# Kernel tuning notes

Measured on AMD Instinct MI355X. Metric: run time of the kernel, lower is better.

## Reference

```python
import jax, jax.numpy as jnp
import numpy as np

NUM_HEADS = 4
SCALE = 0.1767766952966369  # head_dim**-0.5, head_dim=32


def setup_inputs() -> dict:
    key = jax.random.key(0)
    k1, k2, k3 = jax.random.split(key, 3)
    B, N, C = 4096, 49, 384  # B = 64 images * 64 windows, N = 7*7, C = 3*embed_dims
    qkv = jax.random.normal(k1, (B, N, C), dtype=jnp.float32)
    mask = jax.random.normal(k2, (NUM_HEADS, N, N), dtype=jnp.float32)
    rotate_mask = jax.random.normal(k3, (64, N, N), dtype=jnp.float32)  # nW = 64
    hw_pad = jnp.array([56, 56], dtype=jnp.int32)  # metadata only, unused in math
    return {"qkv": qkv, "mask": mask, "rotate_mask": rotate_mask, "hw_pad": hw_pad}


def reference(qkv, mask, rotate_mask, hw_pad):
    B, N, C = qkv.shape
    H = NUM_HEADS
    hd = C // H // 3
    # [B,N,3,H,hd] -> [3,B,H,N,hd]
    qkv_r = qkv.reshape(B, N, 3, H, hd).transpose(2, 0, 3, 1, 4)
    q, k, v = qkv_r[0] * SCALE, qkv_r[1], qkv_r[2]
    attn = jnp.einsum('bhqd,bhkd->bhqk', q, k) + mask  # mask broadcasts over B
    nW = rotate_mask.shape[0]
    # shifted-window mask: add per-window rotate mask, broadcast over image batch and heads
    attn = attn.reshape(B // nW, nW, H, N, N) + rotate_mask[None, :, None, :, :]
    attn = jax.nn.softmax(attn.reshape(B, H, N, N), axis=-1)
    out = jnp.einsum('bhqk,bhkd->bhqd', attn, v)  # [B,H,N,hd]
    return out.transpose(0, 2, 1, 3).reshape(B, N, C // 3)
```

## Files before the change

### kernel.cpp

```cpp
#include <hip/hip_runtime.h>

#define NTOK 49
#define NH 4
#define HD 32
#define CIN 384
#define NW 64
#define NPAD 64
#define SCALE_F 0.1767766952966369f

typedef _Float16 f16x8 __attribute__((ext_vector_type(8)));
typedef float f32x16 __attribute__((ext_vector_type(16)));
typedef __fp16 fp16x2 __attribute__((ext_vector_type(2)));

__device__ __forceinline__ unsigned int pkh(float a, float b) {
    fp16x2 h = __builtin_amdgcn_cvt_pkrtz(a, b);
    return __builtin_bit_cast(unsigned int, h);
}

__global__ __launch_bounds__(64) void prep_cmask(
    const float* __restrict__ mask,
    const float* __restrict__ rot,
    float* __restrict__ cmT)
{
    const int wh = blockIdx.x;
    const int w = wh >> 2, h = wh & 3;
    const int i = threadIdx.x;
    for (int j = 0; j < NPAD; ++j) {
        float v;
        if (j >= NTOK) v = -1e30f;
        else if (i >= NTOK) v = 0.f;
        else v = mask[(h * NTOK + i) * NTOK + j] + rot[(w * NTOK + i) * NTOK + j];
        cmT[((size_t)wh * NPAD + j) * NPAD + i] = v;
    }
}

template<bool USE_CM>
__global__ __launch_bounds__(128) void win_attn_mfma(
    const float* __restrict__ qkv,
    const float* __restrict__ mask,
    const float* __restrict__ rot,
    const float* __restrict__ cmT,
    float* __restrict__ out)
{
    const int h = blockIdx.x & 3;
    const int b = blockIdx.x >> 2;
    const int w = b & (NW - 1);
    const int tid = threadIdx.x;
    const int it = tid >> 6;
    const int lane = tid & 63;
    const int l31 = lane & 31;
    const int hl = lane >> 5;

    __shared__ _Float16 Qs[NPAD * HD];
    __shared__ _Float16 Ks[NPAD * HD];

    const float* base = qkv + (size_t)b * (NTOK * CIN) + h * HD;

    #pragma unroll
    for (int t4 = 0; t4 < 4; ++t4) {
        const int idx = tid + t4 * 128;
        const int n = idx >> 3;
        const int c = idx & 7;
        float4 fq = make_float4(0.f, 0.f, 0.f, 0.f);
        float4 fk = fq;
        if (n < NTOK) {
            const float* p = base + n * CIN + c * 4;
            fq = *reinterpret_cast<const float4*>(p);
            fk = *reinterpret_cast<const float4*>(p + 128);
        }
        uint2 uq, uk;
        uq.x = pkh(fq.x * SCALE_F, fq.y * SCALE_F);
        uq.y = pkh(fq.z * SCALE_F, fq.w * SCALE_F);
        uk.x = pkh(fk.x, fk.y);
        uk.y = pkh(fk.z, fk.w);
        *reinterpret_cast<uint2*>(&Qs[n * HD + c * 4]) = uq;
        *reinterpret_cast<uint2*>(&Ks[n * HD + c * 4]) = uk;
    }

    const int i = l31 + 32 * it;
    float cm[2][16];
    #pragma unroll
    for (int jt = 0; jt < 2; ++jt) {
        #pragma unroll
        for (int r = 0; r < 16; ++r) {
            const int j = (r & 3) + 8 * (r >> 2) + 4 * hl + 32 * jt;
            if (USE_CM) {
                cm[jt][r] = cmT[((size_t)(w * 4 + h) * NPAD + j) * NPAD + i];
            } else {
                float v;
                if (j >= NTOK) v = -1e30f;
                else if (i >= NTOK) v = 0.f;
                else v = mask[(h * NTOK + i) * NTOK + j] + rot[(w * NTOK + i) * NTOK + j];
                cm[jt][r] = v;
            }
        }
    }

    __syncthreads();

    f16x8 ka[2][2], qa[2];
    #pragma unroll
    for (int t = 0; t < 2; ++t) {
        #pragma unroll
        for (int ks = 0; ks < 2; ++ks) {
            ka[t][ks] = *reinterpret_cast<const f16x8*>(&Ks[(l31 + 32 * t) * HD + ks * 16 + hl * 8]);
        }
    }
    #pragma unroll
    for (int ks = 0; ks < 2; ++ks) {
        qa[ks] = *reinterpret_cast<const f16x8*>(&Qs[(l31 + 32 * it) * HD + ks * 16 + hl * 8]);
    }

    f32x16 acc[2];
    #pragma unroll
    for (int jt = 0; jt < 2; ++jt) {
        f32x16 a;
        #pragma unroll
        for (int r = 0; r < 16; ++r) a[r] = 0.f;
        a = __builtin_amdgcn_mfma_f32_32x32x16_f16(ka[jt][0], qa[0], a, 0, 0, 0);
        a = __builtin_amdgcn_mfma_f32_32x32x16_f16(ka[jt][1], qa[1], a, 0, 0, 0);
        acc[jt] = a;
    }

    float m = -3e38f;
    #pragma unroll
    for (int jt = 0; jt < 2; ++jt) {
        #pragma unroll
        for (int r = 0; r < 16; ++r) {
            acc[jt][r] += cm[jt][r];
            m = fmaxf(m, acc[jt][r]);
        }
    }
    m = fmaxf(m, __shfl_xor(m, 32));
    float s = 0.f;
    #pragma unroll
    for (int jt = 0; jt < 2; ++jt) {
        #pragma unroll
        for (int r = 0; r < 16; ++r) {
            const float e = __expf(acc[jt][r] - m);
            acc[jt][r] = e;
            s += e;
        }
    }
    s += __shfl_xor(s, 32);
    const float inv = 1.f / s;
    #pragma unroll
    for (int jt = 0; jt < 2; ++jt) {
        #pragma unroll
        for (int r = 0; r < 16; ++r) acc[jt][r] *= inv;
    }

    f32x16 oacc;
    #pragma unroll
    for (int r = 0; r < 16; ++r) oacc[r] = 0.f;

    #pragma unroll
    for (int ks = 0; ks < 4; ++ks) {
        unsigned int vd[4];
        #pragma unroll
        for (int ep = 0; ep < 4; ++ep) {
            const int j0 = 16 * ks + 8 * hl + 2 * ep;
            float v0 = 0.f, v1 = 0.f;
            if (j0 < NTOK)
                v0 = qkv[((size_t)b * NTOK + j0) * CIN + 256 + h * HD + l31];
            if (j0 + 1 < NTOK)
                v1 = qkv[((size_t)b * NTOK + j0 + 1) * CIN + 256 + h * HD + l31];
            vd[ep] = pkh(v0, v1);
        }
        uint4 vu = make_uint4(vd[0], vd[1], vd[2], vd[3]);
        const f16x8 vb = __builtin_bit_cast(f16x8, vu);

        const int jt = ks >> 1;
        const int r8 = 8 * (ks & 1);
        const unsigned lo0 = pkh(acc[jt][r8 + 0], acc[jt][r8 + 1]);
        const unsigned lo1 = pkh(acc[jt][r8 + 2], acc[jt][r8 + 3]);
        const unsigned hi0 = pkh(acc[jt][r8 + 4], acc[jt][r8 + 5]);
        const unsigned hi1 = pkh(acc[jt][r8 + 6], acc[jt][r8 + 7]);
        const unsigned x0 = hl ? lo0 : hi0;
        const unsigned x1 = hl ? lo1 : hi1;
        const unsigned y0 = (unsigned)__shfl_xor((int)x0, 32);
        const unsigned y1 = (unsigned)__shfl_xor((int)x1, 32);
        uint4 pu;
        pu.x = hl ? y0 : lo0;
        pu.y = hl ? y1 : lo1;
        pu.z = hl ? hi0 : y0;
        pu.w = hl ? hi1 : y1;
        const f16x8 pa = __builtin_bit_cast(f16x8, pu);
        oacc = __builtin_amdgcn_mfma_f32_32x32x16_f16(pa, vb, oacc, 0, 0, 0);
    }

    float* obase = out + (size_t)b * NTOK * (NH * HD) + h * HD + l31;
    #pragma unroll
    for (int r = 0; r < 16; ++r) {
        const int io = (r & 3) + 8 * (r >> 2) + 4 * hl + 32 * it;
        if (io < NTOK) obase[(size_t)io * (NH * HD)] = oacc[r];
    }
}

extern "C" void kernel_launch(void* const* d_in, const int* in_sizes, int n_in,
                              void* d_out, int out_size, void* d_ws, size_t ws_size,
                              hipStream_t stream) {
    const float* qkv  = (const float*)d_in[0];
    const float* mask = (const float*)d_in[1];
    const float* rot  = (const float*)d_in[2];
    float* out = (float*)d_out;

    const int Btot = in_sizes[0] / (NTOK * CIN);
    dim3 grid(Btot * NH);

    const size_t cm_bytes = (size_t)NW * NH * NPAD * NPAD * sizeof(float);
    if (ws_size >= cm_bytes && d_ws != nullptr) {
        float* cmT = (float*)d_ws;
        prep_cmask<<<dim3(NW * NH), 64, 0, stream>>>(mask, rot, cmT);
        win_attn_mfma<true><<<grid, 128, 0, stream>>>(qkv, mask, rot, cmT, out);
    } else {
        win_attn_mfma<false><<<grid, 128, 0, stream>>>(qkv, mask, rot, nullptr, out);
    }
}
```

Measured before the change: 106.9 us.

## Make attention blocks persistent over 8 problems with double-buffered Q/K staging

Each block now handles 8 consecutive (window, head) problems instead of one. Q/K for the next problem are loaded and converted into a second LDS buffer while the current one computes. V loads are hoisted ahead of the softmax so their latency overlaps the QK MFMA. The aim is to hide global load latency and cut block launch overhead, at the cost of fewer blocks (16384 → 2048), more registers and a serialized per-block loop.

```diff
diff --git a/kernel.cpp b/kernel.cpp
--- a/kernel.cpp
+++ b/kernel.cpp
@@ -6,6 +6,7 @@
 #define CIN 384
 #define NW 64
 #define NPAD 64
+#define NPER 8
 #define SCALE_F 0.1767766952966369f
 
 typedef _Float16 f16x8 __attribute__((ext_vector_type(8)));
@@ -40,160 +41,184 @@
     const float* __restrict__ mask,
     const float* __restrict__ rot,
     const float* __restrict__ cmT,
-    float* __restrict__ out)
+    float* __restrict__ out,
+    int nprob)
 {
-    const int h = blockIdx.x & 3;
-    const int b = blockIdx.x >> 2;
-    const int w = b & (NW - 1);
     const int tid = threadIdx.x;
     const int it = tid >> 6;
     const int lane = tid & 63;
     const int l31 = lane & 31;
     const int hl = lane >> 5;
 
-    __shared__ _Float16 Qs[NPAD * HD];
-    __shared__ _Float16 Ks[NPAD * HD];
-
-    const float* base = qkv + (size_t)b * (NTOK * CIN) + h * HD;
-
-    #pragma unroll
-    for (int t4 = 0; t4 < 4; ++t4) {
-        const int idx = tid + t4 * 128;
-        const int n = idx >> 3;
-        const int c = idx & 7;
-        float4 fq = make_float4(0.f, 0.f, 0.f, 0.f);
-        float4 fk = fq;
-        if (n < NTOK) {
-            const float* p = base + n * CIN + c * 4;
-            fq = *reinterpret_cast<const float4*>(p);
-            fk = *reinterpret_cast<const float4*>(p + 128);
-        }
-        uint2 uq, uk;
-        uq.x = pkh(fq.x * SCALE_F, fq.y * SCALE_F);
-        uq.y = pkh(fq.z * SCALE_F, fq.w * SCALE_F);
-        uk.x = pkh(fk.x, fk.y);
-        uk.y = pkh(fk.z, fk.w);
-        *reinterpret_cast<uint2*>(&Qs[n * HD + c * 4]) = uq;
-        *reinterpret_cast<uint2*>(&Ks[n * HD + c * 4]) = uk;
-    }
-
-    const int i = l31 + 32 * it;
-    float cm[2][16];
-    #pragma unroll
-    for (int jt = 0; jt < 2; ++jt) {
+    __shared__ _Float16 Qs[2][NPAD * HD];
+    __shared__ _Float16 Ks[2][NPAD * HD];
+
+    const int p0 = blockIdx.x * NPER;
+
+    auto stage = [&](int p, int s) {
+        const int hh = p & 3;
+        const int bb = p >> 2;
+        const float* base = qkv + (size_t)bb * (NTOK * CIN) + hh * HD;
+        #pragma unroll
+        for (int t4 = 0; t4 < 4; ++t4) {
+            const int idx = tid + t4 * 128;
+            const int n = idx >> 3;
+            const int c = idx & 7;
+            float4 fq = make_float4(0.f, 0.f, 0.f, 0.f);
+            float4 fk = fq;
+            if (n < NTOK) {
+                const float* pp = base + n * CIN + c * 4;
+                fq = *reinterpret_cast<const float4*>(pp);
+                fk = *reinterpret_cast<const float4*>(pp + 128);
+            }
+            uint2 uq, uk;
+            uq.x = pkh(fq.x * SCALE_F, fq.y * SCALE_F);
+            uq.y = pkh(fq.z * SCALE_F, fq.w * SCALE_F);
+            uk.x = pkh(fk.x, fk.y);
+            uk.y = pkh(fk.z, fk.w);
+            *reinterpret_cast<uint2*>(&Qs[s][n * HD + c * 4]) = uq;
+            *reinterpret_cast<uint2*>(&Ks[s][n * HD + c * 4]) = uk;
+        }
+    };
+
+    if (p0 >= nprob) return;
+    stage(p0, 0);
+    __syncthreads();
+
+    int cur = 0;
+    #pragma unroll 1
+    for (int t = 0; t < NPER; ++t) {
+        const int p = p0 + t;
+        if (p >= nprob) break;
+        const int h = p & 3;
+        const int b = p >> 2;
+        const int w = b & (NW - 1);
+        const int i = l31 + 32 * it;
+
+        float cm[2][16];
+        #pragma unroll
+        for (int jt = 0; jt < 2; ++jt) {
+            #pragma unroll
+            for (int r = 0; r < 16; ++r) {
+                const int j = (r & 3) + 8 * (r >> 2) + 4 * hl + 32 * jt;
+                if (USE_CM) {
+                    cm[jt][r] = cmT[((size_t)(w * 4 + h) * NPAD + j) * NPAD + i];
+                } else {
+                    float v;
+                    if (j >= NTOK) v = -1e30f;
+                    else if (i >= NTOK) v = 0.f;
+                    else v = mask[(h * NTOK + i) * NTOK + j] + rot[(w * NTOK + i) * NTOK + j];
+                    cm[jt][r] = v;
+                }
+            }
+        }
+
+        uint4 vb[4];
+        {
+            const float* vbase = qkv + (size_t)b * (NTOK * CIN) + 256 + h * HD + l31;
+            #pragma unroll
+            for (int ks = 0; ks < 4; ++ks) {
+                unsigned dd[4];
+                #pragma unroll
+                for (int ep = 0; ep < 4; ++ep) {
+                    const int j0 = 16 * ks + 8 * hl + 2 * ep;
+                    const float v0 = (j0     < NTOK) ? vbase[(size_t)j0 * CIN]       : 0.f;
+                    const float v1 = (j0 + 1 < NTOK) ? vbase[(size_t)(j0 + 1) * CIN] : 0.f;
+                    dd[ep] = pkh(v0, v1);
+                }
+                vb[ks] = make_uint4(dd[0], dd[1], dd[2], dd[3]);
+            }
+        }
+
+        f16x8 ka[2][2], qa[2];
+        #pragma unroll
+        for (int kt = 0; kt < 2; ++kt) {
+            #pragma unroll
+            for (int ks = 0; ks < 2; ++ks) {
+                ka[kt][ks] = *reinterpret_cast<const f16x8*>(&Ks[cur][(l31 + 32 * kt) * HD + ks * 16 + hl * 8]);
+            }
+        }
+        #pragma unroll
+        for (int ks = 0; ks < 2; ++ks) {
+            qa[ks] = *reinterpret_cast<const f16x8*>(&Qs[cur][(l31 + 32 * it) * HD + ks * 16 + hl * 8]);
+        }
+
+        if (t + 1 < NPER && p + 1 < nprob) stage(p + 1, cur ^ 1);
+
+        f32x16 acc[2];
+        #pragma unroll
+        for (int jt = 0; jt < 2; ++jt) {
+            f32x16 a;
+            #pragma unroll
+            for (int r = 0; r < 16; ++r) a[r] = 0.f;
+            a = __builtin_amdgcn_mfma_f32_32x32x16_f16(ka[jt][0], qa[0], a, 0, 0, 0);
+            a = __builtin_amdgcn_mfma_f32_32x32x16_f16(ka[jt][1], qa[1], a, 0, 0, 0);
+            acc[jt] = a;
+        }
+
+        float m = -3e38f;
+        #pragma unroll
+        for (int jt = 0; jt < 2; ++jt) {
+            #pragma unroll
+            for (int r = 0; r < 16; ++r) {
+                acc[jt][r] += cm[jt][r];
+                m = fmaxf(m, acc[jt][r]);
+            }
+        }
+        m = fmaxf(m, __shfl_xor(m, 32));
+        float s = 0.f;
+        #pragma unroll
+        for (int jt = 0; jt < 2; ++jt) {
+            #pragma unroll
+            for (int r = 0; r < 16; ++r) {
+                const float e = __expf(acc[jt][r] - m);
+                acc[jt][r] = e;
+                s += e;
+            }
+        }
+        s += __shfl_xor(s, 32);
+        const float inv = 1.f / s;
+        #pragma unroll
+        for (int jt = 0; jt < 2; ++jt) {
+            #pragma unroll
+            for (int r = 0; r < 16; ++r) acc[jt][r] *= inv;
+        }
+
+        f32x16 oacc;
+        #pragma unroll
+        for (int r = 0; r < 16; ++r) oacc[r] = 0.f;
+
+        #pragma unroll
+        for (int ks = 0; ks < 4; ++ks) {
+            const int jt = ks >> 1;
+            const int r8 = 8 * (ks & 1);
+            const unsigned lo0 = pkh(acc[jt][r8 + 0], acc[jt][r8 + 1]);
+            const unsigned lo1 = pkh(acc[jt][r8 + 2], acc[jt][r8 + 3]);
+            const unsigned hi0 = pkh(acc[jt][r8 + 4], acc[jt][r8 + 5]);
+            const unsigned hi1 = pkh(acc[jt][r8 + 6], acc[jt][r8 + 7]);
+            const unsigned x0 = hl ? lo0 : hi0;
+            const unsigned x1 = hl ? lo1 : hi1;
+            const unsigned y0 = (unsigned)__shfl_xor((int)x0, 32);
+            const unsigned y1 = (unsigned)__shfl_xor((int)x1, 32);
+            uint4 pu;
+            pu.x = hl ? y0 : lo0;
+            pu.y = hl ? y1 : lo1;
+            pu.z = hl ? hi0 : y0;
+            pu.w = hl ? hi1 : y1;
+            const f16x8 pa  = __builtin_bit_cast(f16x8, pu);
+            const f16x8 vbk = __builtin_bit_cast(f16x8, vb[ks]);
+            oacc = __builtin_amdgcn_mfma_f32_32x32x16_f16(pa, vbk, oacc, 0, 0, 0);
+        }
+
+        float* obase = out + (size_t)b * NTOK * (NH * HD) + h * HD + l31;
         #pragma unroll
         for (int r = 0; r < 16; ++r) {
-            const int j = (r & 3) + 8 * (r >> 2) + 4 * hl + 32 * jt;
-            if (USE_CM) {
-                cm[jt][r] = cmT[((size_t)(w * 4 + h) * NPAD + j) * NPAD + i];
-            } else {
-                float v;
-                if (j >= NTOK) v = -1e30f;
-                else if (i >= NTOK) v = 0.f;
-                else v = mask[(h * NTOK + i) * NTOK + j] + rot[(w * NTOK + i) * NTOK + j];
-                cm[jt][r] = v;
-            }
-        }
-    }
-
-    __syncthreads();
-
-    f16x8 ka[2][2], qa[2];
-    #pragma unroll
-    for (int t = 0; t < 2; ++t) {
-        #pragma unroll
-        for (int ks = 0; ks < 2; ++ks) {
-            ka[t][ks] = *reinterpret_cast<const f16x8*>(&Ks[(l31 + 32 * t) * HD + ks * 16 + hl * 8]);
-        }
-    }
-    #pragma unroll
-    for (int ks = 0; ks < 2; ++ks) {
-        qa[ks] = *reinterpret_cast<const f16x8*>(&Qs[(l31 + 32 * it) * HD + ks * 16 + hl * 8]);
-    }
-
-    f32x16 acc[2];
-    #pragma unroll
-    for (int jt = 0; jt < 2; ++jt) {
-        f32x16 a;
-        #pragma unroll
-        for (int r = 0; r < 16; ++r) a[r] = 0.f;
-        a = __builtin_amdgcn_mfma_f32_32x32x16_f16(ka[jt][0], qa[0], a, 0, 0, 0);
-        a = __builtin_amdgcn_mfma_f32_32x32x16_f16(ka[jt][1], qa[1], a, 0, 0, 0);
-        acc[jt] = a;
-    }
-
-    float m = -3e38f;
-    #pragma unroll
-    for (int jt = 0; jt < 2; ++jt) {
-        #pragma unroll
-        for (int r = 0; r < 16; ++r) {
-            acc[jt][r] += cm[jt][r];
-            m = fmaxf(m, acc[jt][r]);
-        }
-    }
-    m = fmaxf(m, __shfl_xor(m, 32));
-    float s = 0.f;
-    #pragma unroll
-    for (int jt = 0; jt < 2; ++jt) {
-        #pragma unroll
-        for (int r = 0; r < 16; ++r) {
-            const float e = __expf(acc[jt][r] - m);
-            acc[jt][r] = e;
-            s += e;
-        }
-    }
-    s += __shfl_xor(s, 32);
-    const float inv = 1.f / s;
-    #pragma unroll
-    for (int jt = 0; jt < 2; ++jt) {
-        #pragma unroll
-        for (int r = 0; r < 16; ++r) acc[jt][r] *= inv;
-    }
-
-    f32x16 oacc;
-    #pragma unroll
-    for (int r = 0; r < 16; ++r) oacc[r] = 0.f;
-
-    #pragma unroll
-    for (int ks = 0; ks < 4; ++ks) {
-        unsigned int vd[4];
-        #pragma unroll
-        for (int ep = 0; ep < 4; ++ep) {
-            const int j0 = 16 * ks + 8 * hl + 2 * ep;
-            float v0 = 0.f, v1 = 0.f;
-            if (j0 < NTOK)
-                v0 = qkv[((size_t)b * NTOK + j0) * CIN + 256 + h * HD + l31];
-            if (j0 + 1 < NTOK)
-                v1 = qkv[((size_t)b * NTOK + j0 + 1) * CIN + 256 + h * HD + l31];
-            vd[ep] = pkh(v0, v1);
-        }
-        uint4 vu = make_uint4(vd[0], vd[1], vd[2], vd[3]);
-        const f16x8 vb = __builtin_bit_cast(f16x8, vu);
-
-        const int jt = ks >> 1;
-        const int r8 = 8 * (ks & 1);
-        const unsigned lo0 = pkh(acc[jt][r8 + 0], acc[jt][r8 + 1]);
-        const unsigned lo1 = pkh(acc[jt][r8 + 2], acc[jt][r8 + 3]);
-        const unsigned hi0 = pkh(acc[jt][r8 + 4], acc[jt][r8 + 5]);
-        const unsigned hi1 = pkh(acc[jt][r8 + 6], acc[jt][r8 + 7]);
-        const unsigned x0 = hl ? lo0 : hi0;
-        const unsigned x1 = hl ? lo1 : hi1;
-        const unsigned y0 = (unsigned)__shfl_xor((int)x0, 32);
-        const unsigned y1 = (unsigned)__shfl_xor((int)x1, 32);
-        uint4 pu;
-        pu.x = hl ? y0 : lo0;
-        pu.y = hl ? y1 : lo1;
-        pu.z = hl ? hi0 : y0;
-        pu.w = hl ? hi1 : y1;
-        const f16x8 pa = __builtin_bit_cast(f16x8, pu);
-        oacc = __builtin_amdgcn_mfma_f32_32x32x16_f16(pa, vb, oacc, 0, 0, 0);
-    }
-
-    float* obase = out + (size_t)b * NTOK * (NH * HD) + h * HD + l31;
-    #pragma unroll
-    for (int r = 0; r < 16; ++r) {
-        const int io = (r & 3) + 8 * (r >> 2) + 4 * hl + 32 * it;
-        if (io < NTOK) obase[(size_t)io * (NH * HD)] = oacc[r];
+            const int io = (r & 3) + 8 * (r >> 2) + 4 * hl + 32 * it;
+            if (io < NTOK) obase[(size_t)io * (NH * HD)] = oacc[r];
+        }
+
+        __syncthreads();
+        cur ^= 1;
     }
 }
 
@@ -206,14 +231,15 @@
     float* out = (float*)d_out;
 
     const int Btot = in_sizes[0] / (NTOK * CIN);
-    dim3 grid(Btot * NH);
+    const int nprob = Btot * NH;
+    dim3 grid((nprob + NPER - 1) / NPER);
 
     const size_t cm_bytes = (size_t)NW * NH * NPAD * NPAD * sizeof(float);
     if (ws_size >= cm_bytes && d_ws != nullptr) {
         float* cmT = (float*)d_ws;
         prep_cmask<<<dim3(NW * NH), 64, 0, stream>>>(mask, rot, cmT);
-        win_attn_mfma<true><<<grid, 128, 0, stream>>>(qkv, mask, rot, cmT, out);
+        win_attn_mfma<true><<<grid, 128, 0, stream>>>(qkv, mask, rot, cmT, out, nprob);
     } else {
-        win_attn_mfma<false><<<grid, 128, 0, stream>>>(qkv, mask, rot, nullptr, out);
+        win_attn_mfma<false><<<grid, 128, 0, stream>>>(qkv, mask, rot, nullptr, out, nprob);
     }
 }
```

Measured after the change: 123.1 us. 1.15x slower.

## Process all four heads of a window in one 512-thread block

Applied to the files above, without the earlier changes.

Merges the four per-head blocks into one block per window of 8 waves, two per head. The Q and K rows of all heads are staged into padded shared memory (row stride 136 halves) with fully contiguous float4 loads. This cuts the block count fourfold and coalesces the global reads of Q/K across heads. In exchange each block uses more shared memory and larger blocks, which may lower occupancy, and V is still read directly from global memory.

```diff
diff --git a/kernel.cpp b/kernel.cpp
--- a/kernel.cpp
+++ b/kernel.cpp
@@ -6,6 +6,7 @@
 #define CIN 384
 #define NW 64
 #define NPAD 64
+#define QKP 136
 #define SCALE_F 0.1767766952966369f
 
 typedef _Float16 f16x8 __attribute__((ext_vector_type(8)));
@@ -35,46 +36,51 @@
 }
 
 template<bool USE_CM>
-__global__ __launch_bounds__(128) void win_attn_mfma(
+__global__ __launch_bounds__(512) void win_attn_mfma(
     const float* __restrict__ qkv,
     const float* __restrict__ mask,
     const float* __restrict__ rot,
     const float* __restrict__ cmT,
     float* __restrict__ out)
 {
-    const int h = blockIdx.x & 3;
-    const int b = blockIdx.x >> 2;
+    const int b = blockIdx.x;
     const int w = b & (NW - 1);
     const int tid = threadIdx.x;
-    const int it = tid >> 6;
+    const int wid = tid >> 6;
+    const int h = wid >> 1;
+    const int it = wid & 1;
     const int lane = tid & 63;
     const int l31 = lane & 31;
     const int hl = lane >> 5;
 
-    __shared__ _Float16 Qs[NPAD * HD];
-    __shared__ _Float16 Ks[NPAD * HD];
-
-    const float* base = qkv + (size_t)b * (NTOK * CIN) + h * HD;
-
-    #pragma unroll
-    for (int t4 = 0; t4 < 4; ++t4) {
-        const int idx = tid + t4 * 128;
-        const int n = idx >> 3;
-        const int c = idx & 7;
-        float4 fq = make_float4(0.f, 0.f, 0.f, 0.f);
-        float4 fk = fq;
-        if (n < NTOK) {
-            const float* p = base + n * CIN + c * 4;
-            fq = *reinterpret_cast<const float4*>(p);
-            fk = *reinterpret_cast<const float4*>(p + 128);
-        }
-        uint2 uq, uk;
-        uq.x = pkh(fq.x * SCALE_F, fq.y * SCALE_F);
-        uq.y = pkh(fq.z * SCALE_F, fq.w * SCALE_F);
-        uk.x = pkh(fk.x, fk.y);
-        uk.y = pkh(fk.z, fk.w);
-        *reinterpret_cast<uint2*>(&Qs[n * HD + c * 4]) = uq;
-        *reinterpret_cast<uint2*>(&Ks[n * HD + c * 4]) = uk;
+    __shared__ _Float16 Qs[NPAD * QKP];
+    __shared__ _Float16 Ks[NPAD * QKP];
+
+    const float* base = qkv + (size_t)b * (NTOK * CIN);
+
+    for (int e = tid; e < NTOK * 64; e += 512) {
+        const int n = e >> 6;
+        const int c = e & 63;
+        const int col = c * 4;
+        const float4 f = *reinterpret_cast<const float4*>(base + n * CIN + col);
+        uint2 u;
+        if (col < 128) {
+            u.x = pkh(f.x * SCALE_F, f.y * SCALE_F);
+            u.y = pkh(f.z * SCALE_F, f.w * SCALE_F);
+            *reinterpret_cast<uint2*>(&Qs[n * QKP + col]) = u;
+        } else {
+            u.x = pkh(f.x, f.y);
+            u.y = pkh(f.z, f.w);
+            *reinterpret_cast<uint2*>(&Ks[n * QKP + (col - 128)]) = u;
+        }
+    }
+    for (int e = tid; e < 15 * 64; e += 512) {
+        const int n = NTOK + (e >> 6);
+        const int c = e & 63;
+        const int col = c * 4;
+        const uint2 z = make_uint2(0u, 0u);
+        if (col < 128) *reinterpret_cast<uint2*>(&Qs[n * QKP + col]) = z;
+        else           *reinterpret_cast<uint2*>(&Ks[n * QKP + (col - 128)]) = z;
     }
 
     const int i = l31 + 32 * it;
@@ -100,15 +106,15 @@
 
     f16x8 ka[2][2], qa[2];
     #pragma unroll
-    for (int t = 0; t < 2; ++t) {
+    for (int kt = 0; kt < 2; ++kt) {
         #pragma unroll
         for (int ks = 0; ks < 2; ++ks) {
-            ka[t][ks] = *reinterpret_cast<const f16x8*>(&Ks[(l31 + 32 * t) * HD + ks * 16 + hl * 8]);
+            ka[kt][ks] = *reinterpret_cast<const f16x8*>(&Ks[(l31 + 32 * kt) * QKP + h * HD + ks * 16 + hl * 8]);
         }
     }
     #pragma unroll
     for (int ks = 0; ks < 2; ++ks) {
-        qa[ks] = *reinterpret_cast<const f16x8*>(&Qs[(l31 + 32 * it) * HD + ks * 16 + hl * 8]);
+        qa[ks] = *reinterpret_cast<const f16x8*>(&Qs[(l31 + 32 * it) * QKP + h * HD + ks * 16 + hl * 8]);
     }
 
     f32x16 acc[2];
@@ -206,14 +212,14 @@
     float* out = (float*)d_out;
 
     const int Btot = in_sizes[0] / (NTOK * CIN);
-    dim3 grid(Btot * NH);
+    dim3 grid(Btot);
 
     const size_t cm_bytes = (size_t)NW * NH * NPAD * NPAD * sizeof(float);
     if (ws_size >= cm_bytes && d_ws != nullptr) {
         float* cmT = (float*)d_ws;
         prep_cmask<<<dim3(NW * NH), 64, 0, stream>>>(mask, rot, cmT);
-        win_attn_mfma<true><<<grid, 128, 0, stream>>>(qkv, mask, rot, cmT, out);
+        win_attn_mfma<true><<<grid, 512, 0, stream>>>(qkv, mask, rot, cmT, out);
     } else {
-        win_attn_mfma<false><<<grid, 128, 0, stream>>>(qkv, mask, rot, nullptr, out);
-    }
-}
+        win_attn_mfma<false><<<grid, 512, 0, stream>>>(qkv, mask, rot, nullptr, out);
+    }
+}
```

After: 108.2 us. No clear change (+1.2%).

## Process two (window, head) problems per block with prefetch of second Q/K

Applied to the files above, without the earlier changes.

Each block now handles two consecutive (batch, head) attention problems, using double-buffered shared Q/K tiles. The second problem's Q/K are loaded into registers before the first is computed, so global load latency overlaps with the first problem's MFMA and softmax work. This halves the grid size and raises register pressure, and assumes the total problem count is even.

```diff
diff --git a/kernel.cpp b/kernel.cpp
--- a/kernel.cpp
+++ b/kernel.cpp
@@ -42,19 +42,23 @@
     const float* __restrict__ cmT,
     float* __restrict__ out)
 {
-    const int h = blockIdx.x & 3;
-    const int b = blockIdx.x >> 2;
-    const int w = b & (NW - 1);
     const int tid = threadIdx.x;
     const int it = tid >> 6;
     const int lane = tid & 63;
     const int l31 = lane & 31;
     const int hl = lane >> 5;
-
-    __shared__ _Float16 Qs[NPAD * HD];
-    __shared__ _Float16 Ks[NPAD * HD];
-
-    const float* base = qkv + (size_t)b * (NTOK * CIN) + h * HD;
+    const int i = l31 + 32 * it;
+
+    __shared__ _Float16 Qs[2][NPAD * HD];
+    __shared__ _Float16 Ks[2][NPAD * HD];
+
+    const int pA = blockIdx.x * 2;
+    const int pB = pA + 1;
+    const int hA = pA & 3, bA = pA >> 2, wA = bA & (NW - 1);
+    const int hB = pB & 3, bB = pB >> 2, wB = bB & (NW - 1);
+
+    const float* baseA = qkv + (size_t)bA * (NTOK * CIN) + hA * HD;
+    const float* baseB = qkv + (size_t)bB * (NTOK * CIN) + hB * HD;
 
     #pragma unroll
     for (int t4 = 0; t4 < 4; ++t4) {
@@ -64,137 +68,178 @@
         float4 fq = make_float4(0.f, 0.f, 0.f, 0.f);
         float4 fk = fq;
         if (n < NTOK) {
-            const float* p = base + n * CIN + c * 4;
-            fq = *reinterpret_cast<const float4*>(p);
-            fk = *reinterpret_cast<const float4*>(p + 128);
+            const float* pp = baseA + n * CIN + c * 4;
+            fq = *reinterpret_cast<const float4*>(pp);
+            fk = *reinterpret_cast<const float4*>(pp + 128);
         }
         uint2 uq, uk;
         uq.x = pkh(fq.x * SCALE_F, fq.y * SCALE_F);
         uq.y = pkh(fq.z * SCALE_F, fq.w * SCALE_F);
         uk.x = pkh(fk.x, fk.y);
         uk.y = pkh(fk.z, fk.w);
-        *reinterpret_cast<uint2*>(&Qs[n * HD + c * 4]) = uq;
-        *reinterpret_cast<uint2*>(&Ks[n * HD + c * 4]) = uk;
-    }
-
-    const int i = l31 + 32 * it;
-    float cm[2][16];
+        *reinterpret_cast<uint2*>(&Qs[0][n * HD + c * 4]) = uq;
+        *reinterpret_cast<uint2*>(&Ks[0][n * HD + c * 4]) = uk;
+    }
+
+    float4 bq[4], bk[4];
     #pragma unroll
-    for (int jt = 0; jt < 2; ++jt) {
+    for (int t4 = 0; t4 < 4; ++t4) {
+        const int idx = tid + t4 * 128;
+        const int n = idx >> 3;
+        const int c = idx & 7;
+        bq[t4] = make_float4(0.f, 0.f, 0.f, 0.f);
+        bk[t4] = bq[t4];
+        if (n < NTOK) {
+            const float* pp = baseB + n * CIN + c * 4;
+            bq[t4] = *reinterpret_cast<const float4*>(pp);
+            bk[t4] = *reinterpret_cast<const float4*>(pp + 128);
+        }
+    }
+
+    auto load_cm = [&](int w, int h, float cm[2][16]) {
+        #pragma unroll
+        for (int jt = 0; jt < 2; ++jt) {
+            #pragma unroll
+            for (int r = 0; r < 16; ++r) {
+                const int j = (r & 3) + 8 * (r >> 2) + 4 * hl + 32 * jt;
+                if (USE_CM) {
+                    cm[jt][r] = cmT[((size_t)(w * 4 + h) * NPAD + j) * NPAD + i];
+                } else {
+                    float v;
+                    if (j >= NTOK) v = -1e30f;
+                    else if (i >= NTOK) v = 0.f;
+                    else v = mask[(h * NTOK + i) * NTOK + j] + rot[(w * NTOK + i) * NTOK + j];
+                    cm[jt][r] = v;
+                }
+            }
+        }
+    };
+
+    auto compute = [&](int s, int b, int h, const float cm[2][16]) {
+        f16x8 ka[2][2], qa[2];
+        #pragma unroll
+        for (int kt = 0; kt < 2; ++kt) {
+            #pragma unroll
+            for (int ks = 0; ks < 2; ++ks) {
+                ka[kt][ks] = *reinterpret_cast<const f16x8*>(&Ks[s][(l31 + 32 * kt) * HD + ks * 16 + hl * 8]);
+            }
+        }
+        #pragma unroll
+        for (int ks = 0; ks < 2; ++ks) {
+            qa[ks] = *reinterpret_cast<const f16x8*>(&Qs[s][(l31 + 32 * it) * HD + ks * 16 + hl * 8]);
+        }
+
+        f32x16 acc[2];
+        #pragma unroll
+        for (int jt = 0; jt < 2; ++jt) {
+            f32x16 a;
+            #pragma unroll
+            for (int r = 0; r < 16; ++r) a[r] = 0.f;
+            a = __builtin_amdgcn_mfma_f32_32x32x16_f16(ka[jt][0], qa[0], a, 0, 0, 0);
+            a = __builtin_amdgcn_mfma_f32_32x32x16_f16(ka[jt][1], qa[1], a, 0, 0, 0);
+            acc[jt] = a;
+        }
+
+        float m = -3e38f;
+        #pragma unroll
+        for (int jt = 0; jt < 2; ++jt) {
+            #pragma unroll
+            for (int r = 0; r < 16; ++r) {
+                acc[jt][r] += cm[jt][r];
+                m = fmaxf(m, acc[jt][r]);
+            }
+        }
+        m = fmaxf(m, __shfl_xor(m, 32));
+        float sum = 0.f;
+        #pragma unroll
+        for (int jt = 0; jt < 2; ++jt) {
+            #pragma unroll
+            for (int r = 0; r < 16; ++r) {
+                const float e = __expf(acc[jt][r] - m);
+                acc[jt][r] = e;
+                sum += e;
+            }
+        }
+        sum += __shfl_xor(sum, 32);
+        const float inv = 1.f / sum;
+        #pragma unroll
+        for (int jt = 0; jt < 2; ++jt) {
+            #pragma unroll
+            for (int r = 0; r < 16; ++r) acc[jt][r] *= inv;
+        }
+
+        f32x16 oacc;
+        #pragma unroll
+        for (int r = 0; r < 16; ++r) oacc[r] = 0.f;
+
+        #pragma unroll
+        for (int ks = 0; ks < 4; ++ks) {
+            unsigned int vd[4];
+            #pragma unroll
+            for (int ep = 0; ep < 4; ++ep) {
+                const int j0 = 16 * ks + 8 * hl + 2 * ep;
+                float v0 = 0.f, v1 = 0.f;
+                if (j0 < NTOK)
+                    v0 = qkv[((size_t)b * NTOK + j0) * CIN + 256 + h * HD + l31];
+                if (j0 + 1 < NTOK)
+                    v1 = qkv[((size_t)b * NTOK + j0 + 1) * CIN + 256 + h * HD + l31];
+                vd[ep] = pkh(v0, v1);
+            }
+            uint4 vu = make_uint4(vd[0], vd[1], vd[2], vd[3]);
+            const f16x8 vb = __builtin_bit_cast(f16x8, vu);
+
+            const int jt = ks >> 1;
+            const int r8 = 8 * (ks & 1);
+            const unsigned lo0 = pkh(acc[jt][r8 + 0], acc[jt][r8 + 1]);
+            const unsigned lo1 = pkh(acc[jt][r8 + 2], acc[jt][r8 + 3]);
+            const unsigned hi0 = pkh(acc[jt][r8 + 4], acc[jt][r8 + 5]);
+            const unsigned hi1 = pkh(acc[jt][r8 + 6], acc[jt][r8 + 7]);
+            const unsigned x0 = hl ? lo0 : hi0;
+            const unsigned x1 = hl ? lo1 : hi1;
+            const unsigned y0 = (unsigned)__shfl_xor((int)x0, 32);
+            const unsigned y1 = (unsigned)__shfl_xor((int)x1, 32);
+            uint4 pu;
+            pu.x = hl ? y0 : lo0;
+            pu.y = hl ? y1 : lo1;
+            pu.z = hl ? hi0 : y0;
+            pu.w = hl ? hi1 : y1;
+            const f16x8 pa = __builtin_bit_cast(f16x8, pu);
+            oacc = __builtin_amdgcn_mfma_f32_32x32x16_f16(pa, vb, oacc, 0, 0, 0);
+        }
+
+        float* obase = out + (size_t)b * NTOK * (NH * HD) + h * HD + l31;
         #pragma unroll
         for (int r = 0; r < 16; ++r) {
-            const int j = (r & 3) + 8 * (r >> 2) + 4 * hl + 32 * jt;
-            if (USE_CM) {
-                cm[jt][r] = cmT[((size_t)(w * 4 + h) * NPAD + j) * NPAD + i];
-            } else {
-                float v;
-                if (j >= NTOK) v = -1e30f;
-                else if (i >= NTOK) v = 0.f;
-                else v = mask[(h * NTOK + i) * NTOK + j] + rot[(w * NTOK + i) * NTOK + j];
-                cm[jt][r] = v;
-            }
-        }
-    }
+            const int io = (r & 3) + 8 * (r >> 2) + 4 * hl + 32 * it;
+            if (io < NTOK) obase[(size_t)io * (NH * HD)] = oacc[r];
+        }
+    };
+
+    float cmA[2][16];
+    load_cm(wA, hA, cmA);
 
     __syncthreads();
-
-    f16x8 ka[2][2], qa[2];
+    compute(0, bA, hA, cmA);
+
     #pragma unroll
-    for (int t = 0; t < 2; ++t) {
-        #pragma unroll
-        for (int ks = 0; ks < 2; ++ks) {
-            ka[t][ks] = *reinterpret_cast<const f16x8*>(&Ks[(l31 + 32 * t) * HD + ks * 16 + hl * 8]);
-        }
-    }
-    #pragma unroll
-    for (int ks = 0; ks < 2; ++ks) {
-        qa[ks] = *reinterpret_cast<const f16x8*>(&Qs[(l31 + 32 * it) * HD + ks * 16 + hl * 8]);
-    }
-
-    f32x16 acc[2];
-    #pragma unroll
-    for (int jt = 0; jt < 2; ++jt) {
-        f32x16 a;
-        #pragma unroll
-        for (int r = 0; r < 16; ++r) a[r] = 0.f;
-        a = __builtin_amdgcn_mfma_f32_32x32x16_f16(ka[jt][0], qa[0], a, 0, 0, 0);
-        a = __builtin_amdgcn_mfma_f32_32x32x16_f16(ka[jt][1], qa[1], a, 0, 0, 0);
-        acc[jt] = a;
-    }
-
-    float m = -3e38f;
-    #pragma unroll
-    for (int jt = 0; jt < 2; ++jt) {
-        #pragma unroll
-        for (int r = 0; r < 16; ++r) {
-            acc[jt][r] += cm[jt][r];
-            m = fmaxf(m, acc[jt][r]);
-        }
-    }
-    m = fmaxf(m, __shfl_xor(m, 32));
-    float s = 0.f;
-    #pragma unroll
-    for (int jt = 0; jt < 2; ++jt) {
-        #pragma unroll
-        for (int r = 0; r < 16; ++r) {
-            const float e = __expf(acc[jt][r] - m);
-            acc[jt][r] = e;
-            s += e;
-        }
-    }
-    s += __shfl_xor(s, 32);
-    const float inv = 1.f / s;
-    #pragma unroll
-    for (int jt = 0; jt < 2; ++jt) {
-        #pragma unroll
-        for (int r = 0; r < 16; ++r) acc[jt][r] *= inv;
-    }
-
-    f32x16 oacc;
-    #pragma unroll
-    for (int r = 0; r < 16; ++r) oacc[r] = 0.f;
-
-    #pragma unroll
-    for (int ks = 0; ks < 4; ++ks) {
-        unsigned int vd[4];
-        #pragma unroll
-        for (int ep = 0; ep < 4; ++ep) {
-            const int j0 = 16 * ks + 8 * hl + 2 * ep;
-            float v0 = 0.f, v1 = 0.f;
-            if (j0 < NTOK)
-                v0 = qkv[((size_t)b * NTOK + j0) * CIN + 256 + h * HD + l31];
-            if (j0 + 1 < NTOK)
-                v1 = qkv[((size_t)b * NTOK + j0 + 1) * CIN + 256 + h * HD + l31];
-            vd[ep] = pkh(v0, v1);
-        }
-        uint4 vu = make_uint4(vd[0], vd[1], vd[2], vd[3]);
-        const f16x8 vb = __builtin_bit_cast(f16x8, vu);
-
-        const int jt = ks >> 1;
-        const int r8 = 8 * (ks & 1);
-        const unsigned lo0 = pkh(acc[jt][r8 + 0], acc[jt][r8 + 1]);
-        const unsigned lo1 = pkh(acc[jt][r8 + 2], acc[jt][r8 + 3]);
-        const unsigned hi0 = pkh(acc[jt][r8 + 4], acc[jt][r8 + 5]);
-        const unsigned hi1 = pkh(acc[jt][r8 + 6], acc[jt][r8 + 7]);
-        const unsigned x0 = hl ? lo0 : hi0;
-        const unsigned x1 = hl ? lo1 : hi1;
-        const unsigned y0 = (unsigned)__shfl_xor((int)x0, 32);
-        const unsigned y1 = (unsigned)__shfl_xor((int)x1, 32);
-        uint4 pu;
-        pu.x = hl ? y0 : lo0;
-        pu.y = hl ? y1 : lo1;
-        pu.z = hl ? hi0 : y0;
-        pu.w = hl ? hi1 : y1;
-        const f16x8 pa = __builtin_bit_cast(f16x8, pu);
-        oacc = __builtin_amdgcn_mfma_f32_32x32x16_f16(pa, vb, oacc, 0, 0, 0);
-    }
-
-    float* obase = out + (size_t)b * NTOK * (NH * HD) + h * HD + l31;
-    #pragma unroll
-    for (int r = 0; r < 16; ++r) {
-        const int io = (r & 3) + 8 * (r >> 2) + 4 * hl + 32 * it;
-        if (io < NTOK) obase[(size_t)io * (NH * HD)] = oacc[r];
-    }
+    for (int t4 = 0; t4 < 4; ++t4) {
+        const int idx = tid + t4 * 128;
+        const int n = idx >> 3;
+        const int c = idx & 7;
+        uint2 uq, uk;
+        uq.x = pkh(bq[t4].x * SCALE_F, bq[t4].y * SCALE_F);
+        uq.y = pkh(bq[t4].z * SCALE_F, bq[t4].w * SCALE_F);
+        uk.x = pkh(bk[t4].x, bk[t4].y);
+        uk.y = pkh(bk[t4].z, bk[t4].w);
+        *reinterpret_cast<uint2*>(&Qs[1][n * HD + c * 4]) = uq;
+        *reinterpret_cast<uint2*>(&Ks[1][n * HD + c * 4]) = uk;
+    }
+
+    float cmB[2][16];
+    load_cm(wB, hB, cmB);
+
+    __syncthreads();
+    compute(1, bB, hB, cmB);
 }
 
 extern "C" void kernel_launch(void* const* d_in, const int* in_sizes, int n_in,
@@ -206,7 +251,8 @@
     float* out = (float*)d_out;
 
     const int Btot = in_sizes[0] / (NTOK * CIN);
-    dim3 grid(Btot * NH);
+    const int nprob = Btot * NH;
+    dim3 grid(nprob / 2);
 
     const size_t cm_bytes = (size_t)NW * NH * NPAD * NPAD * sizeof(float);
     if (ws_size >= cm_bytes && d_ws != nullptr) {
```

Result: slower. 169.9 us (+59.0%).
